# Kernel tuning notes

Measured on AMD Instinct MI355X. Metric: run time of the kernel, lower is better.

Reference implementation:

```python
import jax, jax.numpy as jnp
import numpy as np

N_NODES = 500000
DIM = 128
L = 5            # walk length (l)
ROW = 16         # l+1 walk entries + 10 negatives
BATCH = 4096


def setup_inputs() -> dict:
    key = jax.random.key(0)
    k1, k2 = jax.random.split(key)
    # kaiming_normal_ on a (n_nodes, dim) tensor: fan_in = dim, std = sqrt(2/fan_in)
    X = jax.random.normal(k1, (N_NODES, DIM), dtype=jnp.float32) * np.sqrt(2.0 / DIM)
    rw_batch = jax.random.randint(k2, (BATCH, ROW), 0, N_NODES, dtype=jnp.int64)
    return {"X": X, "rw_batch": rw_batch, "l": L}


def reference(X, rw_batch, l):
    # X: [N, d] embedding table; rw_batch: [B, L_row] int indices; l: python int
    W = l + 1                      # walk portion length (incl. start node)
    emb = X[rw_batch]              # [B, L_row, d] gather
    start = emb[:, 0]              # [B, d] X_start per walk
    dots = jnp.einsum('bld,bd->bl', emb, start)  # [B, L_row]

    # numerator: sum of dots over walk steps 1..l
    numerator = jnp.sum(dots[:, 1:W], axis=-1)   # [B]

    # dedup of walk indices (set(...) in the original): keep first occurrence only.
    walk = rw_batch[:, :W]                        # [B, W]
    eq = walk[:, :, None] == walk[:, None, :]     # [B, W, W]; eq[b,i,j] = walk_i == walk_j
    prior = np.tril(np.ones((W, W), dtype=bool), -1)  # j < i
    dup = jnp.any(eq & prior[None], axis=-1)      # [B, W] True if seen earlier in walk
    keep = jnp.logical_not(dup).astype(dots.dtype)

    # denominator: exp-dots summed over deduped walk indices + all negative indices
    ex = jnp.exp(dots)                            # [B, L_row]
    denom = jnp.sum(ex[:, :W] * keep, axis=-1) + jnp.sum(ex[:, W:], axis=-1)  # [B]

    loss = l * jnp.log(denom) - numerator         # [B]
    return jnp.mean(loss)
```

## Files before the change

### kernel.cpp

```cpp
#include <hip/hip_runtime.h>
#include <hip/hip_bf16.h>

#define DIM 128
#define ROW 16
#define ROWS_PER_BLOCK 16

__global__ __launch_bounds__(256) void n2v_row_kernel(
    const float* __restrict__ X,
    const int* __restrict__ rw,
    const int* __restrict__ lp,
    float* __restrict__ partial,
    int batch)
{
    const int tid  = threadIdx.x;
    const int g    = tid & 15;
    int row        = blockIdx.x * ROWS_PER_BLOCK + (tid >> 4);
    const bool valid = (row < batch);
    if (!valid) row = batch - 1;

    const int l = *lp;
    const int W = l + 1;

    const int* walk = rw + row * ROW;

    int idx[ROW];
    #pragma unroll
    for (int j = 0; j < ROW; ++j) idx[j] = walk[j];

    float4 a[ROW], b[ROW];
    #pragma unroll
    for (int j = 0; j < ROW; ++j) {
        const float* base = X + (size_t)idx[j] * DIM;
        a[j] = *reinterpret_cast<const float4*>(base + g * 4);
        b[j] = *reinterpret_cast<const float4*>(base + 64 + g * 4);
    }

    const float4 s0 = a[0], s1 = b[0];

    float p[ROW];
    #pragma unroll
    for (int j = 0; j < ROW; ++j) {
        p[j] = a[j].x * s0.x + a[j].y * s0.y + a[j].z * s0.z + a[j].w * s0.w
             + b[j].x * s1.x + b[j].y * s1.y + b[j].z * s1.z + b[j].w * s1.w;
    }

    {
        {
            const bool sel = (g >> 0) & 1;
            float np[8];
            #pragma unroll
            for (int i = 0; i < 8; ++i) {
                float send = sel ? p[i] : p[i + 8];
                float recv = __shfl_xor(send, 1, 64);
                np[i] = (sel ? p[i + 8] : p[i]) + recv;
            }
            #pragma unroll
            for (int i = 0; i < 8; ++i) p[i] = np[i];
        }
        {
            const bool sel = (g >> 1) & 1;
            float np[4];
            #pragma unroll
            for (int i = 0; i < 4; ++i) {
                float send = sel ? p[i] : p[i + 4];
                float recv = __shfl_xor(send, 2, 64);
                np[i] = (sel ? p[i + 4] : p[i]) + recv;
            }
            #pragma unroll
            for (int i = 0; i < 4; ++i) p[i] = np[i];
        }
        {
            const bool sel = (g >> 2) & 1;
            float np[2];
            #pragma unroll
            for (int i = 0; i < 2; ++i) {
                float send = sel ? p[i] : p[i + 2];
                float recv = __shfl_xor(send, 4, 64);
                np[i] = (sel ? p[i + 2] : p[i]) + recv;
            }
            p[0] = np[0]; p[1] = np[1];
        }
        {
            const bool sel = (g >> 3) & 1;
            float send = sel ? p[0] : p[1];
            float recv = __shfl_xor(send, 8, 64);
            p[0] = (sel ? p[1] : p[0]) + recv;
        }
    }

    const int j = ((g & 1) << 3) | ((g & 2) << 1) | ((g & 4) >> 1) | ((g & 8) >> 3);
    const float dot = p[0];

    float numer_c = (j >= 1 && j < W) ? dot : 0.f;
    bool kept = true;
    if (j < W) {
        #pragma unroll
        for (int i = 0; i < ROW; ++i) {
            if (i < j && idx[i] == idx[j]) kept = false;
        }
    }
    float den_c = kept ? expf(dot) : 0.f;

    #pragma unroll
    for (int d = 1; d < 16; d <<= 1) {
        numer_c += __shfl_xor(numer_c, d, 64);
        den_c   += __shfl_xor(den_c, d, 64);
    }

    __shared__ float sm[ROWS_PER_BLOCK];
    if (g == 0) {
        float loss = (float)l * logf(den_c) - numer_c;
        sm[tid >> 4] = valid ? loss : 0.f;
    }
    __syncthreads();
    if (tid == 0) {
        float acc = 0.f;
        #pragma unroll
        for (int i = 0; i < ROWS_PER_BLOCK; ++i) acc += sm[i];
        partial[blockIdx.x] = acc;
    }
}

__global__ __launch_bounds__(64) void n2v_reduce_kernel(
    const float* __restrict__ partial,
    float* __restrict__ out,
    int n, int batch)
{
    const int lane = threadIdx.x;
    float acc = 0.f;
    for (int i = lane; i < n; i += 64) acc += partial[i];
    #pragma unroll
    for (int d = 32; d > 0; d >>= 1) acc += __shfl_xor(acc, d, 64);
    if (lane == 0) out[0] = acc / (float)batch;
}

extern "C" void kernel_launch(void* const* d_in, const int* in_sizes, int n_in,
                              void* d_out, int out_size, void* d_ws, size_t ws_size,
                              hipStream_t stream)
{
    const float* X  = (const float*)d_in[0];
    const int*   rw = (const int*)d_in[1];
    const int*   lp = (const int*)d_in[2];
    float* out = (float*)d_out;

    const int batch = in_sizes[1] / ROW;
    const int grid  = (batch + ROWS_PER_BLOCK - 1) / ROWS_PER_BLOCK;
    float* partial = (float*)d_ws;

    n2v_row_kernel<<<grid, 256, 0, stream>>>(X, rw, lp, partial, batch);
    n2v_reduce_kernel<<<1, 64, 0, stream>>>(partial, out, grid, batch);
}
```

Before: 13.11 us.

## Map one wavefront per walk row with float2 gathers and wider final reduction

Reassigns work so each 64-lane wavefront processes a single row instead of 16 lanes per row, with each lane loading a float2 slice of every gathered embedding. Index loads are vectorized to int4, and the final reduction kernel grows to 256 threads. This raises the grid to 1024 blocks and cuts per-thread registers, aiming for more memory-level parallelism on the random gathers. The cost is extra cross-lane shuffles and redundant index loads across lanes.

```diff
diff --git a/kernel.cpp b/kernel.cpp
--- a/kernel.cpp
+++ b/kernel.cpp
@@ -3,7 +3,7 @@
 
 #define DIM 128
 #define ROW 16
-#define ROWS_PER_BLOCK 16
+#define ROWS_PER_BLOCK 4
 
 __global__ __launch_bounds__(256) void n2v_row_kernel(
     const float* __restrict__ X,
@@ -13,40 +13,45 @@
     int batch)
 {
     const int tid  = threadIdx.x;
-    const int g    = tid & 15;
-    int row        = blockIdx.x * ROWS_PER_BLOCK + (tid >> 4);
+    const int lane = tid & 63;
+    const int wv   = tid >> 6;
+    const int row  = blockIdx.x * ROWS_PER_BLOCK + wv;
     const bool valid = (row < batch);
-    if (!valid) row = batch - 1;
 
     const int l = *lp;
     const int W = l + 1;
 
-    const int* walk = rw + row * ROW;
+    const int* walk = rw + (valid ? row : 0) * ROW;
 
     int idx[ROW];
-    #pragma unroll
-    for (int j = 0; j < ROW; ++j) idx[j] = walk[j];
+    {
+        int4 t0 = *reinterpret_cast<const int4*>(walk);
+        int4 t1 = *reinterpret_cast<const int4*>(walk + 4);
+        int4 t2 = *reinterpret_cast<const int4*>(walk + 8);
+        int4 t3 = *reinterpret_cast<const int4*>(walk + 12);
+        idx[0]=t0.x; idx[1]=t0.y; idx[2]=t0.z; idx[3]=t0.w;
+        idx[4]=t1.x; idx[5]=t1.y; idx[6]=t1.z; idx[7]=t1.w;
+        idx[8]=t2.x; idx[9]=t2.y; idx[10]=t2.z; idx[11]=t2.w;
+        idx[12]=t3.x; idx[13]=t3.y; idx[14]=t3.z; idx[15]=t3.w;
+    }
 
-    float4 a[ROW], b[ROW];
+    float2 e[ROW];
     #pragma unroll
     for (int j = 0; j < ROW; ++j) {
-        const float* base = X + (size_t)idx[j] * DIM;
-        a[j] = *reinterpret_cast<const float4*>(base + g * 4);
-        b[j] = *reinterpret_cast<const float4*>(base + 64 + g * 4);
+        e[j] = *reinterpret_cast<const float2*>(
+            X + (size_t)idx[j] * DIM + lane * 2);
     }
 
-    const float4 s0 = a[0], s1 = b[0];
+    const float2 s = e[0];
 
     float p[ROW];
     #pragma unroll
-    for (int j = 0; j < ROW; ++j) {
-        p[j] = a[j].x * s0.x + a[j].y * s0.y + a[j].z * s0.z + a[j].w * s0.w
-             + b[j].x * s1.x + b[j].y * s1.y + b[j].z * s1.z + b[j].w * s1.w;
-    }
+    for (int j = 0; j < ROW; ++j)
+        p[j] = e[j].x * s.x + e[j].y * s.y;
 
     {
         {
-            const bool sel = (g >> 0) & 1;
+            const bool sel = (lane >> 0) & 1;
             float np[8];
             #pragma unroll
             for (int i = 0; i < 8; ++i) {
@@ -58,7 +63,7 @@
             for (int i = 0; i < 8; ++i) p[i] = np[i];
         }
         {
-            const bool sel = (g >> 1) & 1;
+            const bool sel = (lane >> 1) & 1;
             float np[4];
             #pragma unroll
             for (int i = 0; i < 4; ++i) {
@@ -70,7 +75,7 @@
             for (int i = 0; i < 4; ++i) p[i] = np[i];
         }
         {
-            const bool sel = (g >> 2) & 1;
+            const bool sel = (lane >> 2) & 1;
             float np[2];
             #pragma unroll
             for (int i = 0; i < 2; ++i) {
@@ -81,57 +86,60 @@
             p[0] = np[0]; p[1] = np[1];
         }
         {
-            const bool sel = (g >> 3) & 1;
+            const bool sel = (lane >> 3) & 1;
             float send = sel ? p[0] : p[1];
             float recv = __shfl_xor(send, 8, 64);
             p[0] = (sel ? p[1] : p[0]) + recv;
         }
     }
+    p[0] += __shfl_xor(p[0], 16, 64);
+    p[0] += __shfl_xor(p[0], 32, 64);
 
+    const int g = lane & 15;
     const int j = ((g & 1) << 3) | ((g & 2) << 1) | ((g & 4) >> 1) | ((g & 8) >> 3);
     const float dot = p[0];
 
-    float numer_c = (j >= 1 && j < W) ? dot : 0.f;
-    bool kept = true;
-    if (j < W) {
-        #pragma unroll
-        for (int i = 0; i < ROW; ++i) {
-            if (i < j && idx[i] == idx[j]) kept = false;
+    float numer_c = 0.f, den_c = 0.f;
+    if ((lane >> 4) == 0) {
+        numer_c = (j >= 1 && j < W) ? dot : 0.f;
+        int dup = 0;
+        if (j < W) {
+            const int idxj = walk[j];
+            #pragma unroll
+            for (int i = 0; i < ROW - 1; ++i)
+                dup |= (i < j) & (idx[i] == idxj);
         }
+        den_c = dup ? 0.f : expf(dot);
     }
-    float den_c = kept ? expf(dot) : 0.f;
 
     #pragma unroll
-    for (int d = 1; d < 16; d <<= 1) {
+    for (int d = 1; d < 64; d <<= 1) {
         numer_c += __shfl_xor(numer_c, d, 64);
         den_c   += __shfl_xor(den_c, d, 64);
     }
 
     __shared__ float sm[ROWS_PER_BLOCK];
-    if (g == 0) {
-        float loss = (float)l * logf(den_c) - numer_c;
-        sm[tid >> 4] = valid ? loss : 0.f;
-    }
+    if (lane == 0)
+        sm[wv] = valid ? ((float)l * logf(den_c) - numer_c) : 0.f;
     __syncthreads();
-    if (tid == 0) {
-        float acc = 0.f;
-        #pragma unroll
-        for (int i = 0; i < ROWS_PER_BLOCK; ++i) acc += sm[i];
-        partial[blockIdx.x] = acc;
-    }
+    if (tid == 0)
+        partial[blockIdx.x] = sm[0] + sm[1] + sm[2] + sm[3];
 }
 
-__global__ __launch_bounds__(64) void n2v_reduce_kernel(
+__global__ __launch_bounds__(256) void n2v_reduce_kernel(
     const float* __restrict__ partial,
     float* __restrict__ out,
     int n, int batch)
 {
-    const int lane = threadIdx.x;
     float acc = 0.f;
-    for (int i = lane; i < n; i += 64) acc += partial[i];
+    for (int i = threadIdx.x; i < n; i += 256) acc += partial[i];
     #pragma unroll
-    for (int d = 32; d > 0; d >>= 1) acc += __shfl_xor(acc, d, 64);
-    if (lane == 0) out[0] = acc / (float)batch;
+    for (int d = 1; d < 64; d <<= 1) acc += __shfl_xor(acc, d, 64);
+    __shared__ float sm[4];
+    if ((threadIdx.x & 63) == 0) sm[threadIdx.x >> 6] = acc;
+    __syncthreads();
+    if (threadIdx.x == 0)
+        out[0] = (sm[0] + sm[1] + sm[2] + sm[3]) / (float)batch;
 }
 
 extern "C" void kernel_launch(void* const* d_in, const int* in_sizes, int n_in,
@@ -148,5 +156,5 @@
     float* partial = (float*)d_ws;
 
     n2v_row_kernel<<<grid, 256, 0, stream>>>(X, rw, lp, partial, batch);
-    n2v_reduce_kernel<<<1, 64, 0, stream>>>(partial, out, grid, batch);
+    n2v_reduce_kernel<<<1, 256, 0, stream>>>(partial, out, grid, batch);
 }
```

After: 12.96 us. About the same (-1.1%).
